# Optimization experiments

Hardware: AMD Instinct MI355X
Metric: run time of the kernel (lower is better)

Reference implementation:

```python
import math
import jax, jax.numpy as jnp
import numpy as np

R, N, B, E, H, M = 128, 256, 1, 512, 8, 4
D = E // H
NEG = -1e9  # eye-mask fill value from masked_fill(-1000000000)


def setup_inputs() -> dict:
    key = jax.random.key(0)
    ks = jax.random.split(key, 10)
    p = lambda k, shape: jax.random.normal(k, shape, jnp.float32) * 0.02
    z = lambda n: jnp.zeros((n,), jnp.float32)
    return {
        "x": jax.random.normal(ks[0], (R, N, B, E), jnp.float32),
        "network": jax.random.uniform(ks[1], (B, N, N, M), jnp.float32),
        "Wq": p(ks[2], (E, E)), "bq": z(E),
        "Wk": p(ks[3], (E, E)), "bk": z(E),
        "Wv": p(ks[4], (E, E)), "bv": z(E),
        "Wo": p(ks[5], (E, E)), "bo": z(E),
        "Wq1": p(ks[6], (D, 8)), "bq1": z(8),
        "Wk1": p(ks[7], (1, 8)), "bk1": z(8),
        "l": jax.random.normal(ks[8], (H, 1, 1, 1), jnp.float32),
    }


def reference(x, network, Wq, bq, Wk, bk, Wv, bv, Wo, bo, Wq1, bq1, Wk1, bk1, l):
    # x: [R, N, B, E]; network: [B, N, N, M] (B must be 1, as in the torch module)
    scaling = (D ** -0.5) / math.sqrt(R)  # align_scaling

    q = (x @ Wq + bq).reshape(R, N, B, H, D) * scaling
    k = (x @ Wk + bk).reshape(R, N, B, H, D)

    # shared contraction: summed over rows r, kept per head-dim d -> [H, B, N, N, D]
    qk = jnp.einsum('rinhd,rjnhd->hnijd', q, k)

    # network-bias MLP branch
    q1 = (qk @ Wq1 + bq1).mean(0)                  # [B, N, N, 8]
    network_k = network[..., None] * Wk1[0] + bk1  # Linear(1,8): [B, N, N, M, 8]
    net_attn = jnp.einsum('nijd,nijmd->nijm', q1, network_k)  # [B, N, N, M]
    net_attn = jnp.tile(net_attn, (H, 1, 1, 1))    # repeat over heads (B==1) -> [H, N, N, M]

    # attn_weights 'rinhd,rjnhd->hnij' == qk summed over d
    attn_weights = qk.sum(-1)                      # [H, B, N, N]

    net_probs = jax.nn.softmax(net_attn, axis=-1)  # softmax over M network channels
    net_bias = (network * net_probs).sum(-1)[:, None, :, :]  # [H, 1(B), N, N]
    attn_weights = attn_weights + l * net_bias

    eye = jnp.eye(N, dtype=bool)
    attn_weights = jnp.where(eye, NEG, attn_weights)
    attn_probs = jax.nn.softmax(attn_weights, axis=-1)  # [H, B, N, N]

    v = (x @ Wv + bv).reshape(R, N, B, H, D)
    context = jnp.einsum('hnij,rjnhd->rinhd', attn_probs, v).reshape(R, N, B, E)
    output = context @ Wo + bo
    return (output, attn_probs, l)
```

## Files before the change

### kernel.cpp

```cpp
#include <hip/hip_runtime.h>
#include <hip/hip_bf16.h>
#include <cmath>
#include <stdint.h>

using bf16 = __hip_bfloat16;
typedef __attribute__((ext_vector_type(8))) short bf16x8;
typedef __attribute__((ext_vector_type(4))) float f32x4;

constexpr int LDT  = 40;
constexpr int LDTB = 34;

__device__ __forceinline__ void gload16(const bf16* g, bf16* l)
{
  __builtin_amdgcn_global_load_lds(
      (const __attribute__((address_space(1))) void*)g,
      (__attribute__((address_space(3))) void*)l,
      16, 0, 0);
}

__device__ __forceinline__ int swsrc(int c) { return (((c & 3) ^ ((c >> 3) & 3)) * 8); }

__global__ __launch_bounds__(256)
void k_convert_x(const float* __restrict__ x, bf16* __restrict__ xb)
{
  const long idx = (long)blockIdx.x * 256 + threadIdx.x;
  const float4 f0 = *(const float4*)&x[idx * 8];
  const float4 f1 = *(const float4*)&x[idx * 8 + 4];
  alignas(16) bf16 t[8] = {
    __float2bfloat16(f0.x), __float2bfloat16(f0.y),
    __float2bfloat16(f0.z), __float2bfloat16(f0.w),
    __float2bfloat16(f1.x), __float2bfloat16(f1.y),
    __float2bfloat16(f1.z), __float2bfloat16(f1.w)};
  *(uint4*)&xb[idx * 8] = *(const uint4*)t;
}

__global__ __launch_bounds__(256)
void k_prep_w(const float* __restrict__ Wq, const float* __restrict__ Wk,
              const float* __restrict__ Wv, const float* __restrict__ Wo,
              bf16* __restrict__ WT, float scaling)
{
  const int sel = blockIdx.z;
  const float* W = sel == 0 ? Wq : sel == 1 ? Wk : sel == 2 ? Wv : Wo;
  const float sc = sel == 0 ? scaling : 1.0f;
  const int k0 = blockIdx.x * 64, n0 = blockIdx.y * 64;
  __shared__ float tile[64][68];
  const int tid = threadIdx.x;
  #pragma unroll
  for (int it = 0; it < 4; it++) {
    const int c = tid + it * 256;
    const int kk = c >> 4, nn4 = (c & 15) * 4;
    const float4 v = *(const float4*)&W[(long)(k0 + kk) * 512 + n0 + nn4];
    tile[kk][nn4] = v.x; tile[kk][nn4 + 1] = v.y;
    tile[kk][nn4 + 2] = v.z; tile[kk][nn4 + 3] = v.w;
  }
  __syncthreads();
  #pragma unroll
  for (int it = 0; it < 2; it++) {
    const int c = tid + it * 256;
    const int nn = c >> 3, k8 = (c & 7) * 8;
    alignas(16) bf16 t[8];
    #pragma unroll
    for (int jj = 0; jj < 8; jj++) t[jj] = __float2bfloat16(tile[k8 + jj][nn] * sc);
    *(uint4*)&WT[(long)(sel * 512 + n0 + nn) * 512 + k0 + k8] = *(const uint4*)t;
  }
}

__global__ void k_prep_small(const float* __restrict__ bq, const float* __restrict__ bk,
                             const float* __restrict__ bv, const float* __restrict__ bo,
                             const float* __restrict__ Wq1, const float* __restrict__ Wk1,
                             float* __restrict__ bias_all, float* __restrict__ u, float scaling)
{
  const int idx = blockIdx.x * 256 + threadIdx.x;
  const int s2 = idx >> 9, n2 = idx & 511;
  const float* b = s2 == 0 ? bq : s2 == 1 ? bk : s2 == 2 ? bv : bo;
  bias_all[idx] = b[n2] * (s2 == 0 ? scaling : 1.0f);
  if (idx < 64) {
    float s = 0.0f;
    #pragma unroll
    for (int c = 0; c < 8; c++) s += Wq1[idx * 8 + c] * Wk1[c];
    u[idx] = s;
  }
}

__global__ __launch_bounds__(256)
void gemm_qkv(const bf16* __restrict__ xb, const bf16* __restrict__ WT,
              const float* __restrict__ bias_all,
              bf16* __restrict__ Qn, bf16* __restrict__ Kn, bf16* __restrict__ Vn)
{
  __shared__ bf16 As[3][128 * 32];
  __shared__ bf16 Bs[3][128 * 32];
  const int tid = threadIdx.x, lane = tid & 63;
  const int wid = tid >> 6, wr = wid >> 1, wc = wid & 1;
  const int lr = lane & 15;
  const int lkx = ((lane >> 4) ^ ((lane >> 1) & 3)) * 8;
  const int flat = (blockIdx.x & 7) * 384 + (blockIdx.x >> 3);
  const int m0 = (flat / 12) * 128, n0 = (flat % 12) * 128;
  const int c1 = tid + 256;
  const int ra0 = tid >> 2, ra1 = c1 >> 2;
  const int ps = swsrc(tid);
  f32x4 acc[4][4] = {};

  auto stage = [&](int b, int k0) {
    gload16(&xb[(long)(m0 + ra0) * 512 + k0 + ps], &As[b][tid * 8]);
    gload16(&xb[(long)(m0 + ra1) * 512 + k0 + ps], &As[b][c1 * 8]);
    gload16(&WT[(long)(n0 + ra0) * 512 + k0 + ps], &Bs[b][tid * 8]);
    gload16(&WT[(long)(n0 + ra1) * 512 + k0 + ps], &Bs[b][c1 * 8]);
  };

  stage(0, 0);
  stage(1, 32);

  for (int t = 0; t < 16; ++t) {
    const int cur = t % 3;
    if (t < 14) {
      stage((t + 2) % 3, (t + 2) * 32);
      asm volatile("s_waitcnt vmcnt(8)" ::: "memory");
    } else if (t == 14) {
      asm volatile("s_waitcnt vmcnt(4)" ::: "memory");
    } else {
      asm volatile("s_waitcnt vmcnt(0)" ::: "memory");
    }
    __builtin_amdgcn_s_barrier();
    bf16x8 af[4], bfr[4];
    #pragma unroll
    for (int m = 0; m < 4; m++)
      af[m] = *(const bf16x8*)&As[cur][(wr * 64 + m * 16 + lr) * 32 + lkx];
    #pragma unroll
    for (int n = 0; n < 4; n++)
      bfr[n] = *(const bf16x8*)&Bs[cur][(wc * 64 + n * 16 + lr) * 32 + lkx];
    #pragma unroll
    for (int m = 0; m < 4; m++)
      #pragma unroll
      for (int n = 0; n < 4; n++)
        acc[m][n] = __builtin_amdgcn_mfma_f32_16x16x32_bf16(af[m], bfr[n], acc[m][n], 0, 0, 0);
    __builtin_amdgcn_s_barrier();
  }

  const int er = (lane >> 4) * 4, ec = lane & 15;
  #pragma unroll
  for (int m = 0; m < 4; m++) {
    const int row0 = m0 + wr * 64 + m * 16 + er;
    #pragma unroll
    for (int n = 0; n < 4; n++) {
      const int col = n0 + wc * 64 + n * 16 + ec;
      const float bv = bias_all[col];
      #pragma unroll
      for (int q = 0; q < 4; q++) {
        const float v = acc[m][n][q] + bv;
        const long row = row0 + q;
        if (col < 512)       Qn[row * 512 + col]        = __float2bfloat16(v);
        else if (col < 1024) Kn[row * 512 + col - 512]  = __float2bfloat16(v);
        else                 Vn[row * 512 + col - 1024] = __float2bfloat16(v);
      }
    }
  }
}

__global__ __launch_bounds__(256)
void gemm_logits(const bf16* __restrict__ Qn, const bf16* __restrict__ Kn,
                 const float* __restrict__ u, float* __restrict__ part)
{
  __shared__ bf16 As[3][128 * 32];
  __shared__ bf16 Bs[3][128 * 32];
  __shared__ float us[64];
  const int tid = threadIdx.x, lane = tid & 63;
  const int wid = tid >> 6, wr = wid >> 1, wc = wid & 1;
  const int lr = lane & 15;
  const int lkx = ((lane >> 4) ^ ((lane >> 1) & 3)) * 8;
  const int z = blockIdx.z, batch = z >> 3, ks = z & 7, h = batch & 7;
  const bool uscale = batch >= 8;
  const int m0 = blockIdx.y * 128, n0 = blockIdx.x * 128;
  if (tid < 64) us[tid] = u[tid];
  __syncthreads();
  const int c1 = tid + 256;
  const int ra0 = tid >> 2, ra1 = c1 >> 2;
  const int ps = swsrc(tid);
  f32x4 acc[4][4] = {};

  auto gk_of = [&](int kk) { return ks * 1024 + kk * 32; };

  if (!uscale) {
    auto stage = [&](int b, int kk) {
      const int gk = gk_of(kk), r = gk >> 6, d0 = gk & 63;
      const long ab = (long)(r * 256 + m0) * 512 + h * 64 + d0;
      const long bb = (long)(r * 256 + n0) * 512 + h * 64 + d0;
      gload16(&Qn[ab + (long)ra0 * 512 + ps], &As[b][tid * 8]);
      gload16(&Qn[ab + (long)ra1 * 512 + ps], &As[b][c1 * 8]);
      gload16(&Kn[bb + (long)ra0 * 512 + ps], &Bs[b][tid * 8]);
      gload16(&Kn[bb + (long)ra1 * 512 + ps], &Bs[b][c1 * 8]);
    };
    stage(0, 0);
    stage(1, 1);
    for (int kk = 0; kk < 32; ++kk) {
      const int cur = kk % 3;
      if (kk < 30) {
        stage((kk + 2) % 3, kk + 2);
        asm volatile("s_waitcnt vmcnt(8)" ::: "memory");
      } else if (kk == 30) {
        asm volatile("s_waitcnt vmcnt(4)" ::: "memory");
      } else {
        asm volatile("s_waitcnt vmcnt(0)" ::: "memory");
      }
      __builtin_amdgcn_s_barrier();
      bf16x8 af[4], bfr[4];
      #pragma unroll
      for (int m = 0; m < 4; m++)
        af[m] = *(const bf16x8*)&As[cur][(wr * 64 + m * 16 + lr) * 32 + lkx];
      #pragma unroll
      for (int n = 0; n < 4; n++)
        bfr[n] = *(const bf16x8*)&Bs[cur][(wc * 64 + n * 16 + lr) * 32 + lkx];
      #pragma unroll
      for (int m = 0; m < 4; m++)
        #pragma unroll
        for (int n = 0; n < 4; n++)
          acc[m][n] = __builtin_amdgcn_mfma_f32_16x16x32_bf16(af[m], bfr[n], acc[m][n], 0, 0, 0);
      __builtin_amdgcn_s_barrier();
    }
  } else {
    {
      const int gk = gk_of(0), r = gk >> 6, d0 = gk & 63;
      const long ab = (long)(r * 256 + m0) * 512 + h * 64 + d0;
      const long bb = (long)(r * 256 + n0) * 512 + h * 64 + d0;
      gload16(&Kn[bb + (long)ra0 * 512 + ps], &Bs[0][tid * 8]);
      gload16(&Kn[bb + (long)ra1 * 512 + ps], &Bs[0][c1 * 8]);
      const uint4 v0 = *(const uint4*)&Qn[ab + (long)ra0 * 512 + ps];
      const uint4 v1 = *(const uint4*)&Qn[ab + (long)ra1 * 512 + ps];
      const unsigned short* p0 = (const unsigned short*)&v0;
      const unsigned short* p1 = (const unsigned short*)&v1;
      alignas(16) bf16 t0[8], t1[8];
      #pragma unroll
      for (int jj = 0; jj < 8; jj++) {
        t0[jj] = __float2bfloat16(__bfloat162float(*(const bf16*)&p0[jj]) * us[d0 + ps + jj]);
        t1[jj] = __float2bfloat16(__bfloat162float(*(const bf16*)&p1[jj]) * us[d0 + ps + jj]);
      }
      *(uint4*)&As[0][tid * 8] = *(const uint4*)t0;
      *(uint4*)&As[0][c1 * 8] = *(const uint4*)t1;
    }
    __syncthreads();
    int buf = 0;
    for (int kk = 0; kk < 32; ++kk) {
      uint4 va0, va1;
      int d0n = 0;
      if (kk < 31) {
        const int gk = gk_of(kk + 1), r = gk >> 6;
        d0n = gk & 63;
        const long ab = (long)(r * 256 + m0) * 512 + h * 64 + d0n;
        const long bb = (long)(r * 256 + n0) * 512 + h * 64 + d0n;
        gload16(&Kn[bb + (long)ra0 * 512 + ps], &Bs[buf ^ 1][tid * 8]);
        gload16(&Kn[bb + (long)ra1 * 512 + ps], &Bs[buf ^ 1][c1 * 8]);
        va0 = *(const uint4*)&Qn[ab + (long)ra0 * 512 + ps];
        va1 = *(const uint4*)&Qn[ab + (long)ra1 * 512 + ps];
      }
      bf16x8 af[4], bfr[4];
      #pragma unroll
      for (int m = 0; m < 4; m++)
        af[m] = *(const bf16x8*)&As[buf][(wr * 64 + m * 16 + lr) * 32 + lkx];
      #pragma unroll
      for (int n = 0; n < 4; n++)
        bfr[n] = *(const bf16x8*)&Bs[buf][(wc * 64 + n * 16 + lr) * 32 + lkx];
      #pragma unroll
      for (int m = 0; m < 4; m++)
        #pragma unroll
        for (int n = 0; n < 4; n++)
          acc[m][n] = __builtin_amdgcn_mfma_f32_16x16x32_bf16(af[m], bfr[n], acc[m][n], 0, 0, 0);
      if (kk < 31) {
        const unsigned short* p0 = (const unsigned short*)&va0;
        const unsigned short* p1 = (const unsigned short*)&va1;
        alignas(16) bf16 t0[8], t1[8];
        #pragma unroll
        for (int jj = 0; jj < 8; jj++) {
          t0[jj] = __float2bfloat16(__bfloat162float(*(const bf16*)&p0[jj]) * us[d0n + ps + jj]);
          t1[jj] = __float2bfloat16(__bfloat162float(*(const bf16*)&p1[jj]) * us[d0n + ps + jj]);
        }
        *(uint4*)&As[buf ^ 1][tid * 8] = *(const uint4*)t0;
        *(uint4*)&As[buf ^ 1][c1 * 8] = *(const uint4*)t1;
      }
      __syncthreads();
      buf ^= 1;
    }
  }

  float* C = part + (long)z * 65536;
  const int er = (lane >> 4) * 4, ec = lane & 15;
  #pragma unroll
  for (int m = 0; m < 4; m++)
    #pragma unroll
    for (int n = 0; n < 4; n++) {
      const int col = n0 + wc * 64 + n * 16 + ec;
      #pragma unroll
      for (int q = 0; q < 4; q++)
        C[(long)(m0 + wr * 64 + m * 16 + er + q) * 256 + col] = acc[m][n][q];
    }
}

__global__ __launch_bounds__(128)
void gemm_ctx(const bf16* __restrict__ Pb, const bf16* __restrict__ Vn,
              bf16* __restrict__ ctxb)
{
  __shared__ bf16 As[128 * LDT];
  __shared__ bf16 Bs[64 * LDTB];
  const int m0 = blockIdx.x * 128, r = blockIdx.y, h = blockIdx.z;
  const int tid = threadIdx.x, lane = tid & 63, wid = tid >> 6;
  const int wr = wid;
  const int lr = lane & 15, lk = (lane >> 4) * 8;
  const bf16* A = Pb + (long)h * 65536;
  f32x4 acc[4][4] = {};

  for (int j0 = 0; j0 < 256; j0 += 32) {
    #pragma unroll
    for (int c = tid; c < 512; c += 128) {
      const int row = c >> 2, k8 = (c & 3) * 8;
      *(uint4*)&As[row * LDT + k8] = *(const uint4*)&A[(long)(m0 + row) * 256 + j0 + k8];
    }
    #pragma unroll
    for (int c = tid; c < 256; c += 128) {
      const int jj = c >> 3, d8 = (c & 7) * 8;
      const uint4 v = *(const uint4*)&Vn[((long)(r * 256 + j0 + jj)) * 512 + h * 64 + d8];
      const unsigned short* pv = (const unsigned short*)&v;
      #pragma unroll
      for (int t = 0; t < 8; t++)
        *(unsigned short*)&Bs[(d8 + t) * LDTB + jj] = pv[t];
    }
    __syncthreads();
    bf16x8 af[4], bfr[4];
    #pragma unroll
    for (int m = 0; m < 4; m++)
      af[m] = *(const bf16x8*)&As[(wr * 64 + m * 16 + lr) * LDT + lk];
    #pragma unroll
    for (int n = 0; n < 4; n++)
      bfr[n] = *(const bf16x8*)&Bs[(n * 16 + lr) * LDTB + lk];
    #pragma unroll
    for (int m = 0; m < 4; m++)
      #pragma unroll
      for (int n = 0; n < 4; n++)
        acc[m][n] = __builtin_amdgcn_mfma_f32_16x16x32_bf16(af[m], bfr[n], acc[m][n], 0, 0, 0);
    __syncthreads();
  }

  const int er = (lane >> 4) * 4, ec = lane & 15;
  #pragma unroll
  for (int m = 0; m < 4; m++) {
    const int i0 = m0 + wr * 64 + m * 16 + er;
    #pragma unroll
    for (int n = 0; n < 4; n++) {
      const int d = n * 16 + ec;
      #pragma unroll
      for (int q = 0; q < 4; q++)
        ctxb[((long)(r * 256 + i0 + q)) * 512 + h * 64 + d] = __float2bfloat16(acc[m][n][q]);
    }
  }
}

__global__ __launch_bounds__(512)
void gemm_outp(const bf16* __restrict__ A, const bf16* __restrict__ B,
               float* __restrict__ C, const float* __restrict__ bias)
{
  __shared__ bf16 As[3][128 * 32];
  __shared__ bf16 Bs[3][256 * 32];
  const int tid = threadIdx.x, lane = tid & 63, wid = tid >> 6;
  const int wr = wid >> 2, wc = wid & 3;
  const int lr = lane & 15;
  const int lkx = ((lane >> 4) ^ ((lane >> 1) & 3)) * 8;
  const int m0 = blockIdx.y * 128, n0 = blockIdx.x * 256;
  const int ra = tid >> 2;
  const int cb1 = tid + 512;
  const int rb0 = tid >> 2, rb1 = cb1 >> 2;
  const int ps = swsrc(tid);
  f32x4 acc[4][4] = {};

  auto stage = [&](int b, int k0) {
    gload16(&A[(long)(m0 + ra) * 512 + k0 + ps], &As[b][tid * 8]);
    gload16(&B[(long)(n0 + rb0) * 512 + k0 + ps], &Bs[b][tid * 8]);
    gload16(&B[(long)(n0 + rb1) * 512 + k0 + ps], &Bs[b][cb1 * 8]);
  };

  stage(0, 0);
  stage(1, 32);

  for (int t = 0; t < 16; ++t) {
    const int cur = t % 3;
    if (t < 14) {
      stage((t + 2) % 3, (t + 2) * 32);
      asm volatile("s_waitcnt vmcnt(6)" ::: "memory");
    } else if (t == 14) {
      asm volatile("s_waitcnt vmcnt(3)" ::: "memory");
    } else {
      asm volatile("s_waitcnt vmcnt(0)" ::: "memory");
    }
    __builtin_amdgcn_s_barrier();
    bf16x8 af[4], bfr[4];
    #pragma unroll
    for (int m = 0; m < 4; m++)
      af[m] = *(const bf16x8*)&As[cur][(wr * 64 + m * 16 + lr) * 32 + lkx];
    #pragma unroll
    for (int n = 0; n < 4; n++)
      bfr[n] = *(const bf16x8*)&Bs[cur][(wc * 64 + n * 16 + lr) * 32 + lkx];
    #pragma unroll
    for (int m = 0; m < 4; m++)
      #pragma unroll
      for (int n = 0; n < 4; n++)
        acc[m][n] = __builtin_amdgcn_mfma_f32_16x16x32_bf16(af[m], bfr[n], acc[m][n], 0, 0, 0);
    __builtin_amdgcn_s_barrier();
  }

  const int er = (lane >> 4) * 4, ec = lane & 15;
  #pragma unroll
  for (int m = 0; m < 4; m++) {
    const int row0 = m0 + wr * 64 + m * 16 + er;
    #pragma unroll
    for (int n = 0; n < 4; n++) {
      const int col = n0 + wc * 64 + n * 16 + ec;
      const float bv = bias[col];
      #pragma unroll
      for (int q = 0; q < 4; q++)
        C[(long)(row0 + q) * 512 + col] = acc[m][n][q] + bv;
    }
  }
}

__global__ void k_bias(const float* __restrict__ part, const float* __restrict__ network,
                       const float* __restrict__ bq1, const float* __restrict__ Wk1,
                       float* __restrict__ net_bias)
{
  const int i = blockIdx.x, j = threadIdx.x;
  float c1 = 0.0f;
  #pragma unroll
  for (int c = 0; c < 8; c++) c1 += bq1[c] * Wk1[c];
  float s1 = 0.0f;
  const long ij = i * 256 + j;
  #pragma unroll
  for (int s = 64; s < 128; s++) s1 += part[(long)s * 65536 + ij];
  s1 = 0.125f * s1 + c1;
  const float4 nw = *(const float4*)&network[ij * 4];
  const float a0 = nw.x * s1, a1 = nw.y * s1, a2 = nw.z * s1, a3 = nw.w * s1;
  const float mx = fmaxf(fmaxf(a0, a1), fmaxf(a2, a3));
  const float e0 = expf(a0 - mx), e1 = expf(a1 - mx), e2 = expf(a2 - mx), e3 = expf(a3 - mx);
  const float inv = 1.0f / (e0 + e1 + e2 + e3);
  net_bias[ij] = (nw.x * e0 + nw.y * e1 + nw.z * e2 + nw.w * e3) * inv;
}

__global__ void k_softmax(const float* __restrict__ part, const float* __restrict__ net_bias,
                          const float* __restrict__ l, float* __restrict__ out_probs,
                          bf16* __restrict__ Pb, float* __restrict__ out_l)
{
  const int i = blockIdx.x, h = blockIdx.y, j = threadIdx.x;
  const long ij = i * 256 + j;
  float w = 0.0f;
  #pragma unroll
  for (int ks = 0; ks < 8; ks++) w += part[(long)(h * 8 + ks) * 65536 + ij];
  w += l[h] * net_bias[ij];
  if (j == i) w = -1e9f;
  float m = w;
  #pragma unroll
  for (int o = 32; o; o >>= 1) m = fmaxf(m, __shfl_xor(m, o));
  __shared__ float red[4], red2[4];
  if ((j & 63) == 0) red[j >> 6] = m;
  __syncthreads();
  m = fmaxf(fmaxf(red[0], red[1]), fmaxf(red[2], red[3]));
  const float e = expf(w - m);
  float s = e;
  #pragma unroll
  for (int o = 32; o; o >>= 1) s += __shfl_xor(s, o);
  if ((j & 63) == 0) red2[j >> 6] = s;
  __syncthreads();
  s = red2[0] + red2[1] + red2[2] + red2[3];
  const float p = e / s;
  out_probs[(long)h * 65536 + ij] = p;
  Pb[(long)h * 65536 + ij] = __float2bfloat16(p);
  if (h == 0 && i == 0 && j < 8) out_l[j] = l[j];
}

extern "C" void kernel_launch(void* const* d_in, const int* in_sizes, int n_in,
                              void* d_out, int out_size, void* d_ws, size_t ws_size,
                              hipStream_t stream)
{
  const float* x   = (const float*)d_in[0];
  const float* net = (const float*)d_in[1];
  const float* Wq  = (const float*)d_in[2];
  const float* bq  = (const float*)d_in[3];
  const float* Wk  = (const float*)d_in[4];
  const float* bk  = (const float*)d_in[5];
  const float* Wv  = (const float*)d_in[6];
  const float* bv  = (const float*)d_in[7];
  const float* Wo  = (const float*)d_in[8];
  const float* bo  = (const float*)d_in[9];
  const float* Wq1 = (const float*)d_in[10];
  const float* bq1 = (const float*)d_in[11];
  const float* Wk1 = (const float*)d_in[12];
  const float* l   = (const float*)d_in[14];
  float* out = (float*)d_out;

  bf16* Qn = (bf16*)d_out;
  bf16* Kn = Qn + 16777216;

  char* ws = (char*)d_ws;
  size_t off = 0;
  auto alloc = [&](size_t bytes) { char* p = ws + off; off += (bytes + 255) & ~255ULL; return p; };
  bf16*  WT       = (bf16*)alloc(2048ULL * 512 * 2);
  float* bias_all = (float*)alloc(2048 * 4);
  float* u        = (float*)alloc(64 * 4);
  bf16*  xb       = (bf16*)alloc(16777216ULL * 2);
  bf16*  Vn       = (bf16*)alloc(16777216ULL * 2);
  float* net_bias = (float*)alloc(65536ULL * 4);
  bf16*  Pb       = (bf16*)alloc(8ULL * 65536 * 2);
  float* part     = (float*)xb;
  bf16*  ctxb     = xb;

  const float scaling = (float)(0.125 / sqrt(128.0));

  k_convert_x<<<8192, 256, 0, stream>>>(x, xb);
  k_prep_w<<<dim3(8, 8, 4), 256, 0, stream>>>(Wq, Wk, Wv, Wo, WT, scaling);
  k_prep_small<<<8, 256, 0, stream>>>(bq, bk, bv, bo, Wq1, Wk1, bias_all, u, scaling);

  gemm_qkv<<<3072, 256, 0, stream>>>(xb, WT, bias_all, Qn, Kn, Vn);

  gemm_logits<<<dim3(2, 2, 128), 256, 0, stream>>>(Qn, Kn, u, part);

  k_bias<<<256, 256, 0, stream>>>(part, net, bq1, Wk1, net_bias);
  k_softmax<<<dim3(256, 8, 1), 256, 0, stream>>>(part, net_bias, l,
                                                 out + 16777216, Pb, out + 17301504);

  gemm_ctx<<<dim3(2, 128, 8), 128, 0, stream>>>(Pb, Vn, ctxb);

  gemm_outp<<<dim3(2, 256, 1), 512, 0, stream>>>(ctxb, WT + 1536 * 512, out, bias_all + 1536);
}
```

Measured before the change: 223.3 us.

## Store V transposed per head from QKV epilogue and pipeline context GEMM

New measurement: 204.3 us. 1.09x faster.

```diff
diff --git a/kernel.cpp b/kernel.cpp
--- a/kernel.cpp
+++ b/kernel.cpp
@@ -7,8 +7,7 @@
 typedef __attribute__((ext_vector_type(8))) short bf16x8;
 typedef __attribute__((ext_vector_type(4))) float f32x4;
 
-constexpr int LDT  = 40;
-constexpr int LDTB = 34;
+constexpr long HS = 2097152;
 
 __device__ __forceinline__ void gload16(const bf16* g, bf16* l)
 {
@@ -85,10 +84,11 @@
 __global__ __launch_bounds__(256)
 void gemm_qkv(const bf16* __restrict__ xb, const bf16* __restrict__ WT,
               const float* __restrict__ bias_all,
-              bf16* __restrict__ Qn, bf16* __restrict__ Kn, bf16* __restrict__ Vn)
-{
-  __shared__ bf16 As[3][128 * 32];
-  __shared__ bf16 Bs[3][128 * 32];
+              bf16* __restrict__ Qn, bf16* __restrict__ Kn, bf16* __restrict__ Vj)
+{
+  __shared__ __align__(16) unsigned short smem[24576];
+  bf16* As = (bf16*)smem;
+  bf16* Bs = (bf16*)smem + 12288;
   const int tid = threadIdx.x, lane = tid & 63;
   const int wid = tid >> 6, wr = wid >> 1, wc = wid & 1;
   const int lr = lane & 15;
@@ -101,10 +101,10 @@
   f32x4 acc[4][4] = {};
 
   auto stage = [&](int b, int k0) {
-    gload16(&xb[(long)(m0 + ra0) * 512 + k0 + ps], &As[b][tid * 8]);
-    gload16(&xb[(long)(m0 + ra1) * 512 + k0 + ps], &As[b][c1 * 8]);
-    gload16(&WT[(long)(n0 + ra0) * 512 + k0 + ps], &Bs[b][tid * 8]);
-    gload16(&WT[(long)(n0 + ra1) * 512 + k0 + ps], &Bs[b][c1 * 8]);
+    gload16(&xb[(long)(m0 + ra0) * 512 + k0 + ps], &As[b * 4096 + tid * 8]);
+    gload16(&xb[(long)(m0 + ra1) * 512 + k0 + ps], &As[b * 4096 + c1 * 8]);
+    gload16(&WT[(long)(n0 + ra0) * 512 + k0 + ps], &Bs[b * 4096 + tid * 8]);
+    gload16(&WT[(long)(n0 + ra1) * 512 + k0 + ps], &Bs[b * 4096 + c1 * 8]);
   };
 
   stage(0, 0);
@@ -124,10 +124,10 @@
     bf16x8 af[4], bfr[4];
     #pragma unroll
     for (int m = 0; m < 4; m++)
-      af[m] = *(const bf16x8*)&As[cur][(wr * 64 + m * 16 + lr) * 32 + lkx];
+      af[m] = *(const bf16x8*)&As[cur * 4096 + (wr * 64 + m * 16 + lr) * 32 + lkx];
     #pragma unroll
     for (int n = 0; n < 4; n++)
-      bfr[n] = *(const bf16x8*)&Bs[cur][(wc * 64 + n * 16 + lr) * 32 + lkx];
+      bfr[n] = *(const bf16x8*)&Bs[cur * 4096 + (wc * 64 + n * 16 + lr) * 32 + lkx];
     #pragma unroll
     for (int m = 0; m < 4; m++)
       #pragma unroll
@@ -137,21 +137,49 @@
   }
 
   const int er = (lane >> 4) * 4, ec = lane & 15;
-  #pragma unroll
-  for (int m = 0; m < 4; m++) {
-    const int row0 = m0 + wr * 64 + m * 16 + er;
-    #pragma unroll
-    for (int n = 0; n < 4; n++) {
-      const int col = n0 + wc * 64 + n * 16 + ec;
-      const float bv = bias_all[col];
-      #pragma unroll
-      for (int q = 0; q < 4; q++) {
-        const float v = acc[m][n][q] + bv;
-        const long row = row0 + q;
-        if (col < 512)       Qn[row * 512 + col]        = __float2bfloat16(v);
-        else if (col < 1024) Kn[row * 512 + col - 512]  = __float2bfloat16(v);
-        else                 Vn[row * 512 + col - 1024] = __float2bfloat16(v);
+  if (n0 < 1024) {
+    #pragma unroll
+    for (int m = 0; m < 4; m++) {
+      const int row0 = m0 + wr * 64 + m * 16 + er;
+      #pragma unroll
+      for (int n = 0; n < 4; n++) {
+        const int col = n0 + wc * 64 + n * 16 + ec;
+        const float bv = bias_all[col];
+        #pragma unroll
+        for (int q = 0; q < 4; q++) {
+          const float v = acc[m][n][q] + bv;
+          const long row = row0 + q;
+          if (col < 512) Qn[row * 512 + col]       = __float2bfloat16(v);
+          else           Kn[row * 512 + col - 512] = __float2bfloat16(v);
+        }
       }
+    }
+  } else {
+    bf16* vt = (bf16*)smem;
+    #pragma unroll
+    for (int m = 0; m < 4; m++) {
+      const int rt0 = wr * 64 + m * 16 + er;
+      #pragma unroll
+      for (int n = 0; n < 4; n++) {
+        const int ct = wc * 64 + n * 16 + ec;
+        const float bv = bias_all[n0 + ct];
+        #pragma unroll
+        for (int q = 0; q < 4; q++)
+          vt[(rt0 + q) * 140 + ct] = __float2bfloat16(acc[m][n][q] + bv);
+      }
+    }
+    __syncthreads();
+    const int r = m0 >> 8, tok0 = m0 & 255;
+    #pragma unroll
+    for (int cc = 0; cc < 8; cc++) {
+      const int c = cc * 256 + tid;
+      const int ct2 = c & 127, i8 = (c >> 7) * 8;
+      alignas(16) bf16 tmp[8];
+      #pragma unroll
+      for (int t = 0; t < 8; t++) tmp[t] = vt[(i8 + t) * 140 + ct2];
+      const int hd = n0 - 1024 + ct2;
+      const int h = hd >> 6, d = hd & 63;
+      *(uint4*)&Vj[(long)h * HS + (long)(r * 64 + d) * 256 + tok0 + i8] = *(const uint4*)tmp;
     }
   }
 }
@@ -293,48 +321,58 @@
     }
 }
 
-__global__ __launch_bounds__(128)
-void gemm_ctx(const bf16* __restrict__ Pb, const bf16* __restrict__ Vn,
+__global__ __launch_bounds__(256)
+void gemm_ctx(const bf16* __restrict__ Pb, const bf16* __restrict__ Vj,
               bf16* __restrict__ ctxb)
 {
-  __shared__ bf16 As[128 * LDT];
-  __shared__ bf16 Bs[64 * LDTB];
-  const int m0 = blockIdx.x * 128, r = blockIdx.y, h = blockIdx.z;
-  const int tid = threadIdx.x, lane = tid & 63, wid = tid >> 6;
-  const int wr = wid;
-  const int lr = lane & 15, lk = (lane >> 4) * 8;
+  __shared__ bf16 As[3][128 * 32];
+  __shared__ bf16 Bs[3][128 * 32];
+  const int tid = threadIdx.x, lane = tid & 63;
+  const int wid = tid >> 6, wr = wid >> 1, wc = wid & 1;
+  const int lr = lane & 15;
+  const int lkx = ((lane >> 4) ^ ((lane >> 1) & 3)) * 8;
+  const int m0 = blockIdx.y * 128, n0 = blockIdx.x * 128, h = blockIdx.z;
   const bf16* A = Pb + (long)h * 65536;
+  const bf16* B = Vj + (long)h * HS;
+  const int c1 = tid + 256;
+  const int ra0 = tid >> 2, ra1 = c1 >> 2;
+  const int ps = swsrc(tid);
   f32x4 acc[4][4] = {};
 
-  for (int j0 = 0; j0 < 256; j0 += 32) {
-    #pragma unroll
-    for (int c = tid; c < 512; c += 128) {
-      const int row = c >> 2, k8 = (c & 3) * 8;
-      *(uint4*)&As[row * LDT + k8] = *(const uint4*)&A[(long)(m0 + row) * 256 + j0 + k8];
-    }
-    #pragma unroll
-    for (int c = tid; c < 256; c += 128) {
-      const int jj = c >> 3, d8 = (c & 7) * 8;
-      const uint4 v = *(const uint4*)&Vn[((long)(r * 256 + j0 + jj)) * 512 + h * 64 + d8];
-      const unsigned short* pv = (const unsigned short*)&v;
-      #pragma unroll
-      for (int t = 0; t < 8; t++)
-        *(unsigned short*)&Bs[(d8 + t) * LDTB + jj] = pv[t];
-    }
-    __syncthreads();
+  auto stage = [&](int b, int k0) {
+    gload16(&A[(long)(m0 + ra0) * 256 + k0 + ps], &As[b][tid * 8]);
+    gload16(&A[(long)(m0 + ra1) * 256 + k0 + ps], &As[b][c1 * 8]);
+    gload16(&B[(long)(n0 + ra0) * 256 + k0 + ps], &Bs[b][tid * 8]);
+    gload16(&B[(long)(n0 + ra1) * 256 + k0 + ps], &Bs[b][c1 * 8]);
+  };
+
+  stage(0, 0);
+  stage(1, 32);
+
+  for (int t = 0; t < 8; ++t) {
+    const int cur = t % 3;
+    if (t < 6) {
+      stage((t + 2) % 3, (t + 2) * 32);
+      asm volatile("s_waitcnt vmcnt(8)" ::: "memory");
+    } else if (t == 6) {
+      asm volatile("s_waitcnt vmcnt(4)" ::: "memory");
+    } else {
+      asm volatile("s_waitcnt vmcnt(0)" ::: "memory");
+    }
+    __builtin_amdgcn_s_barrier();
     bf16x8 af[4], bfr[4];
     #pragma unroll
     for (int m = 0; m < 4; m++)
-      af[m] = *(const bf16x8*)&As[(wr * 64 + m * 16 + lr) * LDT + lk];
+      af[m] = *(const bf16x8*)&As[cur][(wr * 64 + m * 16 + lr) * 32 + lkx];
     #pragma unroll
     for (int n = 0; n < 4; n++)
-      bfr[n] = *(const bf16x8*)&Bs[(n * 16 + lr) * LDTB + lk];
+      bfr[n] = *(const bf16x8*)&Bs[cur][(wc * 64 + n * 16 + lr) * 32 + lkx];
     #pragma unroll
     for (int m = 0; m < 4; m++)
       #pragma unroll
       for (int n = 0; n < 4; n++)
         acc[m][n] = __builtin_amdgcn_mfma_f32_16x16x32_bf16(af[m], bfr[n], acc[m][n], 0, 0, 0);
-    __syncthreads();
+    __builtin_amdgcn_s_barrier();
   }
 
   const int er = (lane >> 4) * 4, ec = lane & 15;
@@ -343,10 +381,11 @@
     const int i0 = m0 + wr * 64 + m * 16 + er;
     #pragma unroll
     for (int n = 0; n < 4; n++) {
-      const int d = n * 16 + ec;
+      const int col = n0 + wc * 64 + n * 16 + ec;
+      const int rr = col >> 6, dd = col & 63;
       #pragma unroll
       for (int q = 0; q < 4; q++)
-        ctxb[((long)(r * 256 + i0 + q)) * 512 + h * 64 + d] = __float2bfloat16(acc[m][n][q]);
+        ctxb[(long)(rr * 256 + i0 + q) * 512 + h * 64 + dd] = __float2bfloat16(acc[m][n][q]);
     }
   }
 }
@@ -500,7 +539,7 @@
   float* bias_all = (float*)alloc(2048 * 4);
   float* u        = (float*)alloc(64 * 4);
   bf16*  xb       = (bf16*)alloc(16777216ULL * 2);
-  bf16*  Vn       = (bf16*)alloc(16777216ULL * 2);
+  bf16*  Vj       = (bf16*)alloc(16777216ULL * 2);
   float* net_bias = (float*)alloc(65536ULL * 4);
   bf16*  Pb       = (bf16*)alloc(8ULL * 65536 * 2);
   float* part     = (float*)xb;
@@ -512,7 +551,7 @@
   k_prep_w<<<dim3(8, 8, 4), 256, 0, stream>>>(Wq, Wk, Wv, Wo, WT, scaling);
   k_prep_small<<<8, 256, 0, stream>>>(bq, bk, bv, bo, Wq1, Wk1, bias_all, u, scaling);
 
-  gemm_qkv<<<3072, 256, 0, stream>>>(xb, WT, bias_all, Qn, Kn, Vn);
+  gemm_qkv<<<3072, 256, 0, stream>>>(xb, WT, bias_all, Qn, Kn, Vj);
 
   gemm_logits<<<dim3(2, 2, 128), 256, 0, stream>>>(Qn, Kn, u, part);
 
@@ -520,7 +559,7 @@
   k_softmax<<<dim3(256, 8, 1), 256, 0, stream>>>(part, net_bias, l,
                                                  out + 16777216, Pb, out + 17301504);
 
-  gemm_ctx<<<dim3(2, 128, 8), 128, 0, stream>>>(Pb, Vn, ctxb);
+  gemm_ctx<<<dim3(64, 2, 8), 256, 0, stream>>>(Pb, Vj, ctxb);
 
   gemm_outp<<<dim3(2, 256, 1), 512, 0, stream>>>(ctxb, WT + 1536 * 512, out, bias_all + 1536);
 }
```
